# Kernel optimization log

Hardware: AMD Instinct MI355X
Metric: run time of the kernel (lower is better)

The kernel has to match this reference:

```python
import jax, jax.numpy as jnp
import numpy as np

N_NODES = 262144
N_EDGES = 524288
N_GRAPHS = 8192
BN_EPS = 1e-5


def setup_inputs() -> dict:
    key = jax.random.key(0)
    ks = jax.random.split(key, 12)
    x = jax.random.normal(ks[0], (N_NODES, 77), dtype=jnp.float32)
    edge_index = jax.random.randint(ks[1], (2, N_EDGES), 0, N_NODES, dtype=jnp.int32)
    # sorted segment ids covering every graph (arange-style fill)
    batch = (jnp.arange(N_NODES, dtype=jnp.int32) * N_GRAPHS // N_NODES).astype(jnp.int32)
    s77 = 1.0 / np.sqrt(77.0)
    s128 = 1.0 / np.sqrt(128.0)
    return {
        "x": x,
        "edge_index": edge_index,
        "batch": batch,
        "w0a": jax.random.normal(ks[2], (77, 128), dtype=jnp.float32) * s77,
        "b0a": jnp.zeros((128,), jnp.float32),
        "w0b": jax.random.normal(ks[3], (128, 128), dtype=jnp.float32) * s128,
        "b0b": jnp.zeros((128,), jnp.float32),
        "wa": jax.random.normal(ks[4], (4, 128, 128), dtype=jnp.float32) * s128,
        "ba": jnp.zeros((4, 128), jnp.float32),
        "wb": jax.random.normal(ks[5], (4, 128, 128), dtype=jnp.float32) * s128,
        "bb": jnp.zeros((4, 128), jnp.float32),
        "gamma": jnp.ones((5, 128), jnp.float32),
        "beta": jnp.zeros((5, 128), jnp.float32),
    }


def _gin_encoder(x, edge_index, batch, w0a, b0a, w0b, b0b, wa, ba, wb, bb, gamma, beta):
    n = x.shape[0]
    src, dst = edge_index[0], edge_index[1]
    h = x
    pooled = []
    for i in range(5):
        # GINConv (eps=0): agg_i = h_i + sum_{(j,i) in E} h_j, then 2-layer MLP
        agg = h + jax.ops.segment_sum(h[src], dst, num_segments=n)
        if i == 0:
            w1, c1, w2, c2 = w0a, b0a, w0b, b0b
        else:
            w1, c1, w2, c2 = wa[i - 1], ba[i - 1], wb[i - 1], bb[i - 1]
        h = jax.nn.relu(agg @ w1 + c1) @ w2 + c2
        h = jax.nn.relu(h)
        # BatchNorm1d (training-mode batch statistics, biased variance)
        mean = jnp.mean(h, axis=0)
        var = jnp.mean(jnp.square(h - mean), axis=0)
        h = gamma[i] * (h - mean) * jax.lax.rsqrt(var + BN_EPS) + beta[i]
        pooled.append(jax.ops.segment_max(h, batch, num_segments=N_GRAPHS))
    return jnp.concatenate(pooled, axis=1)  # [N_GRAPHS, 640]


def reference(x, edge_index, batch, w0a, b0a, w0b, b0b, wa, ba, wb, bb, gamma, beta):
    return _gin_encoder(x, edge_index, batch, w0a, b0a, w0b, b0b, wa, ba, wb, bb, gamma, beta)
```

## Files before the change

kernel.cpp:

```cpp
#include <hip/hip_runtime.h>
#include <cstdint>
#include <cstddef>

#define N_NODES_C 262144
#define N_EDGES_C 524288
#define N_GRAPHS_C 8192
#define BN_EPS_C 1e-5f

typedef short short8 __attribute__((ext_vector_type(8)));
typedef float f32x4 __attribute__((ext_vector_type(4)));

__device__ __forceinline__ unsigned short f2bf(float f) {
  unsigned int u = __float_as_uint(f);
  u += 0x7fffu + ((u >> 16) & 1u);
  return (unsigned short)(u >> 16);
}
__device__ __forceinline__ float bf2f(unsigned short h) {
  return __uint_as_float(((unsigned int)h) << 16);
}

__global__ __launch_bounds__(256) void hist_kernel(const int* __restrict__ dst, int* __restrict__ cnt) {
  int e = blockIdx.x * 256 + threadIdx.x;
  if (e < N_EDGES_C) atomicAdd(&cnt[dst[e]], 1);
}

__global__ __launch_bounds__(256) void scanA_kernel(const int* __restrict__ cnt,
                                                    int* __restrict__ rs, int* __restrict__ bsums) {
  __shared__ int lds[256];
  const int b = blockIdx.x, t = threadIdx.x;
  int4 v = ((const int4*)(cnt + b * 1024))[t];
  lds[t] = v.x + v.y + v.z + v.w;
  __syncthreads();
  for (int off = 1; off < 256; off <<= 1) {
    int add = (t >= off) ? lds[t - off] : 0;
    __syncthreads();
    lds[t] += add;
    __syncthreads();
  }
  int excl = (t > 0) ? lds[t - 1] : 0;
  if (t == 255) bsums[b] = lds[255];
  int4 o;
  o.x = excl; o.y = excl + v.x; o.z = excl + v.x + v.y; o.w = excl + v.x + v.y + v.z;
  ((int4*)(rs + b * 1024))[t] = o;
}

__global__ __launch_bounds__(256) void scanB_kernel(int* __restrict__ bsums) {
  __shared__ int lds[256];
  const int t = threadIdx.x;
  lds[t] = bsums[t];
  __syncthreads();
  for (int off = 1; off < 256; off <<= 1) {
    int add = (t >= off) ? lds[t - off] : 0;
    __syncthreads();
    lds[t] += add;
    __syncthreads();
  }
  bsums[t] = (t > 0) ? lds[t - 1] : 0;
}

__global__ __launch_bounds__(256) void scanC_kernel(int* __restrict__ rs, int* __restrict__ cursor,
                                                    const int* __restrict__ bsums) {
  int i = blockIdx.x * 256 + threadIdx.x;
  int v = rs[i] + bsums[i >> 10];
  rs[i] = v;
  cursor[i] = v;
  if (i == 0) rs[N_NODES_C] = N_EDGES_C;
}

__global__ __launch_bounds__(256) void edge_bucket_kernel(const int* __restrict__ src,
                                                          const int* __restrict__ dst,
                                                          int* __restrict__ cursor,
                                                          int* __restrict__ ebuf) {
  int e = blockIdx.x * 256 + threadIdx.x;
  if (e >= N_EDGES_C) return;
  int pos = atomicAdd(&cursor[dst[e]], 1);
  ebuf[pos] = src[e];
}

__global__ __launch_bounds__(256) void agg128_kernel(const float4* __restrict__ h4,
                                                     const int* __restrict__ rs,
                                                     const int* __restrict__ ebuf,
                                                     float4* __restrict__ agg4) {
  int idx = blockIdx.x * 256 + threadIdx.x;
  int n = idx >> 5, q = idx & 31;
  int s = rs[n], e = rs[n + 1];
  float4 v = h4[(size_t)n * 32 + q];
  for (int i = s; i < e; ++i) {
    int srcn = ebuf[i];
    float4 u = h4[(size_t)srcn * 32 + q];
    v.x += u.x; v.y += u.y; v.z += u.z; v.w += u.w;
  }
  agg4[(size_t)n * 32 + q] = v;
}

__global__ __launch_bounds__(256) void agg77_kernel(const float* __restrict__ x,
                                                    const int* __restrict__ rs,
                                                    const int* __restrict__ ebuf,
                                                    float* __restrict__ agg) {
  int idx = blockIdx.x * 256 + threadIdx.x;
  int n = idx >> 5, q = idx & 31;
  int s = rs[n], e = rs[n + 1];
  const size_t nb = (size_t)n * 77;
  float v0 = x[nb + q];
  float v1 = x[nb + q + 32];
  float v2 = (q < 13) ? x[nb + q + 64] : 0.f;
  for (int i = s; i < e; ++i) {
    const size_t sb = (size_t)ebuf[i] * 77;
    v0 += x[sb + q];
    v1 += x[sb + q + 32];
    if (q < 13) v2 += x[sb + q + 64];
  }
  const size_t ob = (size_t)n * 128;
  agg[ob + q] = v0;
  agg[ob + q + 32] = v1;
  agg[ob + q + 64] = (q < 13) ? v2 : 0.f;
  agg[ob + q + 96] = 0.f;
}

__global__ __launch_bounds__(256) void wsplit_kernel(const float* __restrict__ w0a,
                                                     const float* __restrict__ w0b,
                                                     const float* __restrict__ wa,
                                                     const float* __restrict__ wb,
                                                     unsigned short* __restrict__ Whi,
                                                     unsigned short* __restrict__ Wlo) {
  int tid = blockIdx.x * 256 + threadIdx.x;
  int mat = tid >> 11;
  int rem = tid & 2047;
  int ct = rem >> 8;
  int ks = (rem >> 6) & 3;
  int lane = rem & 63;
  const int c = ct * 16 + (lane & 15);
  const size_t base = (size_t)mat * 16384 + (size_t)((ct * 4 + ks) * 64 + lane) * 8;
#pragma unroll
  for (int j = 0; j < 8; ++j) {
    int k = ks * 32 + ((lane >> 4) << 3) + j;
    float w;
    if (mat == 0)      w = (k < 77) ? w0a[k * 128 + c] : 0.f;
    else if (mat == 1) w = w0b[k * 128 + c];
    else if (mat < 6)  w = wa[(size_t)(mat - 2) * 16384 + k * 128 + c];
    else               w = wb[(size_t)(mat - 6) * 16384 + k * 128 + c];
    unsigned short h = f2bf(w);
    Whi[base + j] = h;
    Wlo[base + j] = f2bf(w - bf2f(h));
  }
}

template <bool STATS>
__global__ __launch_bounds__(256) void gemm_kernel(const float* __restrict__ A,
                                                   const unsigned short* __restrict__ Whi,
                                                   const unsigned short* __restrict__ Wlo,
                                                   const float* __restrict__ bias,
                                                   float* __restrict__ C,
                                                   float* __restrict__ stats) {
  __shared__ float bsum[128];
  __shared__ float bsq[128];
  const int t = threadIdx.x;
  const int lane = t & 63;
  const int wv = t >> 6;
  if (STATS) {
    if (t < 128) { bsum[t] = 0.f; bsq[t] = 0.f; }
    __syncthreads();
  }

  const size_t strip = (size_t)blockIdx.x * 64 + wv * 16;
  const size_t rowA = strip + (lane & 15);
  const int kb = (lane >> 4) << 3;
  const float* Arow = A + rowA * 128 + kb;

  const short8* Bh = (const short8*)Whi;
  const short8* Bl = (const short8*)Wlo;

  f32x4 acc[8] = {};

#pragma unroll
  for (int ks = 0; ks < 4; ++ks) {
    f32x4 a0 = *(const f32x4*)(Arow + ks * 32);
    f32x4 a1 = *(const f32x4*)(Arow + ks * 32 + 4);
    short8 ah, al;
#pragma unroll
    for (int j = 0; j < 8; ++j) {
      float f = (j < 4) ? a0[j] : a1[j - 4];
      unsigned short h = f2bf(f);
      ah[j] = (short)h;
      al[j] = (short)f2bf(f - bf2f(h));
    }
#pragma unroll
    for (int ct = 0; ct < 8; ++ct) {
      const int idx = (ct * 4 + ks) * 64 + lane;
      short8 wh = Bh[idx];
      short8 wl = Bl[idx];
      acc[ct] = __builtin_amdgcn_mfma_f32_16x16x32_bf16(ah, wh, acc[ct], 0, 0, 0);
      acc[ct] = __builtin_amdgcn_mfma_f32_16x16x32_bf16(al, wh, acc[ct], 0, 0, 0);
      acc[ct] = __builtin_amdgcn_mfma_f32_16x16x32_bf16(ah, wl, acc[ct], 0, 0, 0);
    }
  }

  const int cbase = lane & 15;
  const size_t rowD = strip + ((lane >> 4) << 2);
#pragma unroll
  for (int ct = 0; ct < 8; ++ct) {
    const int c = ct * 16 + cbase;
    const float bc = bias[c];
    float s = 0.f, q = 0.f;
#pragma unroll
    for (int j = 0; j < 4; ++j) {
      float v = fmaxf(acc[ct][j] + bc, 0.f);
      C[(rowD + j) * 128 + c] = v;
      s += v;
      q += v * v;
    }
    if (STATS) {
      atomicAdd(&bsum[c], s);
      atomicAdd(&bsq[c], q);
    }
  }

  if (STATS) {
    __syncthreads();
    if (t < 128) {
      atomicAdd(&stats[t], bsum[t]);
      atomicAdd(&stats[128 + t], bsq[t]);
    }
  }
}

__global__ __launch_bounds__(256) void bn_pool_kernel(float* __restrict__ h,
                                                      const float* __restrict__ stats,
                                                      const float* __restrict__ gamma,
                                                      const float* __restrict__ beta,
                                                      float* __restrict__ out, int layer) {
  __shared__ float red[256];
  const int g = blockIdx.x;
  const int t = threadIdx.x;
  const int f = t & 127, half = t >> 7;

  const float inv_n = 1.0f / (float)N_NODES_C;
  float mean = stats[f] * inv_n;
  float var = stats[128 + f] * inv_n - mean * mean;
  float sc = gamma[layer * 128 + f] * rsqrtf(var + BN_EPS_C);
  float sh = beta[layer * 128 + f] - mean * sc;

  float m = -3.4e38f;
  size_t base = ((size_t)g * 32 + half * 16) * 128 + f;
#pragma unroll
  for (int r = 0; r < 16; ++r) {
    float v = h[base + (size_t)r * 128];
    v = v * sc + sh;
    h[base + (size_t)r * 128] = v;
    m = fmaxf(m, v);
  }
  red[t] = m;
  __syncthreads();
  if (t < 128) out[(size_t)g * 640 + layer * 128 + f] = fmaxf(red[t], red[t + 128]);
}

extern "C" void kernel_launch(void* const* d_in, const int* in_sizes, int n_in,
                              void* d_out, int out_size, void* d_ws, size_t ws_size,
                              hipStream_t stream) {
  const float* x = (const float*)d_in[0];
  const int* ei = (const int*)d_in[1];
  const int* src = ei;
  const int* dst = ei + N_EDGES_C;
  const float* w0a = (const float*)d_in[3];
  const float* b0a = (const float*)d_in[4];
  const float* w0b = (const float*)d_in[5];
  const float* b0b = (const float*)d_in[6];
  const float* wa = (const float*)d_in[7];
  const float* ba = (const float*)d_in[8];
  const float* wb = (const float*)d_in[9];
  const float* bb = (const float*)d_in[10];
  const float* gamma = (const float*)d_in[11];
  const float* beta = (const float*)d_in[12];
  float* out = (float*)d_out;

  const size_t NNf = (size_t)N_NODES_C * 128;
  float* ws = (float*)d_ws;
  float* H = ws;
  float* AGG = ws + NNf;
  float* STATS = ws + 2 * NNf;
  int* cnt = (int*)(STATS + 256);
  int* rowstart = cnt + N_NODES_C;
  int* cursor = rowstart + N_NODES_C + 4;
  int* bsums = cursor + N_NODES_C;
  int* ebuf = bsums + 256;
  unsigned short* Whi = (unsigned short*)(((uintptr_t)(ebuf + N_EDGES_C) + 15) & ~(uintptr_t)15);
  unsigned short* Wlo = Whi + (size_t)10 * 16384;

  wsplit_kernel<<<80, 256, 0, stream>>>(w0a, w0b, wa, wb, Whi, Wlo);
  hipMemsetAsync(cnt, 0, N_NODES_C * sizeof(int), stream);
  hist_kernel<<<N_EDGES_C / 256, 256, 0, stream>>>(dst, cnt);
  scanA_kernel<<<256, 256, 0, stream>>>(cnt, rowstart, bsums);
  scanB_kernel<<<1, 256, 0, stream>>>(bsums);
  scanC_kernel<<<N_NODES_C / 256, 256, 0, stream>>>(rowstart, cursor, bsums);
  edge_bucket_kernel<<<N_EDGES_C / 256, 256, 0, stream>>>(src, dst, cursor, ebuf);

  const int GB = N_NODES_C / 64;

  agg77_kernel<<<(N_NODES_C * 32) / 256, 256, 0, stream>>>(x, rowstart, ebuf, AGG);
  gemm_kernel<false><<<GB, 256, 0, stream>>>(AGG, Whi, Wlo, b0a, AGG, nullptr);
  hipMemsetAsync(STATS, 0, 256 * sizeof(float), stream);
  gemm_kernel<true><<<GB, 256, 0, stream>>>(AGG, Whi + 16384, Wlo + 16384, b0b, H, STATS);
  bn_pool_kernel<<<N_GRAPHS_C, 256, 0, stream>>>(H, STATS, gamma, beta, out, 0);

  for (int i = 1; i < 5; ++i) {
    agg128_kernel<<<(N_NODES_C * 32) / 256, 256, 0, stream>>>((const float4*)H, rowstart, ebuf,
                                                              (float4*)AGG);
    const size_t mA = (size_t)(2 + (i - 1)) * 16384;
    const size_t mB = (size_t)(6 + (i - 1)) * 16384;
    gemm_kernel<false><<<GB, 256, 0, stream>>>(AGG, Whi + mA, Wlo + mA,
                                               ba + (size_t)(i - 1) * 128, AGG, nullptr);
    hipMemsetAsync(STATS, 0, 256 * sizeof(float), stream);
    gemm_kernel<true><<<GB, 256, 0, stream>>>(AGG, Whi + mB, Wlo + mB,
                                              bb + (size_t)(i - 1) * 128, H, STATS);
    bn_pool_kernel<<<N_GRAPHS_C, 256, 0, stream>>>(H, STATS, gamma, beta, out, i);
  }
}
```

Baseline: 1.941 ms.

## Stage split-bf16 weights in LDS and process 512 rows per GEMM block

The GEMM kernel now copies the hi/lo bf16 weight matrices into 64 KB of shared memory once per block, instead of reading them from global or L2 for every 16-row strip. Each block covers 512 rows over four sub-blocks, with two 16-row tiles per wave so each weight fragment feeds six MFMAs. Batch-norm sums are kept in registers across the whole block and flushed once to shared and then global atomics, cutting atomic traffic. The trade-off is a grid of only 512 blocks and heavy LDS use, which lowers occupancy and latency hiding in this mostly bandwidth-bound GEMM.

```diff
diff --git a/kernel.cpp b/kernel.cpp
--- a/kernel.cpp
+++ b/kernel.cpp
@@ -152,70 +152,97 @@
                                                    const float* __restrict__ bias,
                                                    float* __restrict__ C,
                                                    float* __restrict__ stats) {
+  __shared__ int4 sW[4096];
   __shared__ float bsum[128];
   __shared__ float bsq[128];
+
   const int t = threadIdx.x;
   const int lane = t & 63;
   const int wv = t >> 6;
+
+  const int4* WhG = (const int4*)Whi;
+  const int4* WlG = (const int4*)Wlo;
+#pragma unroll
+  for (int i = 0; i < 8; ++i) sW[t + i * 256] = WhG[t + i * 256];
+#pragma unroll
+  for (int i = 0; i < 8; ++i) sW[2048 + t + i * 256] = WlG[t + i * 256];
+  __syncthreads();
+  const short8* sWh = (const short8*)sW;
+  const short8* sWl = (const short8*)(sW + 2048);
+
+  const int cbase = lane & 15;
+  const int kb = (lane >> 4) << 3;
+
+  float bc[8];
+#pragma unroll
+  for (int ct = 0; ct < 8; ++ct) bc[ct] = bias[ct * 16 + cbase];
+
+  float ssum[8] = {}, ssq[8] = {};
+
+  for (int sblk = 0; sblk < 4; ++sblk) {
+    const size_t strip = (size_t)blockIdx.x * 512 + sblk * 128 + wv * 32;
+    const float* Ar0 = A + (strip + cbase) * 128 + kb;
+    const float* Ar1 = Ar0 + 16 * 128;
+
+    f32x4 acc[2][8] = {};
+
+#pragma unroll
+    for (int ks = 0; ks < 4; ++ks) {
+      f32x4 a00 = *(const f32x4*)(Ar0 + ks * 32);
+      f32x4 a01 = *(const f32x4*)(Ar0 + ks * 32 + 4);
+      f32x4 a10 = *(const f32x4*)(Ar1 + ks * 32);
+      f32x4 a11 = *(const f32x4*)(Ar1 + ks * 32 + 4);
+      short8 ah0, al0, ah1, al1;
+#pragma unroll
+      for (int j = 0; j < 8; ++j) {
+        float f0 = (j < 4) ? a00[j] : a01[j - 4];
+        unsigned short h0 = f2bf(f0);
+        ah0[j] = (short)h0;
+        al0[j] = (short)f2bf(f0 - bf2f(h0));
+        float f1 = (j < 4) ? a10[j] : a11[j - 4];
+        unsigned short h1 = f2bf(f1);
+        ah1[j] = (short)h1;
+        al1[j] = (short)f2bf(f1 - bf2f(h1));
+      }
+#pragma unroll
+      for (int ct = 0; ct < 8; ++ct) {
+        const int idx = (ct * 4 + ks) * 64 + lane;
+        short8 wh = sWh[idx];
+        short8 wl = sWl[idx];
+        acc[0][ct] = __builtin_amdgcn_mfma_f32_16x16x32_bf16(ah0, wh, acc[0][ct], 0, 0, 0);
+        acc[0][ct] = __builtin_amdgcn_mfma_f32_16x16x32_bf16(al0, wh, acc[0][ct], 0, 0, 0);
+        acc[0][ct] = __builtin_amdgcn_mfma_f32_16x16x32_bf16(ah0, wl, acc[0][ct], 0, 0, 0);
+        acc[1][ct] = __builtin_amdgcn_mfma_f32_16x16x32_bf16(ah1, wh, acc[1][ct], 0, 0, 0);
+        acc[1][ct] = __builtin_amdgcn_mfma_f32_16x16x32_bf16(al1, wh, acc[1][ct], 0, 0, 0);
+        acc[1][ct] = __builtin_amdgcn_mfma_f32_16x16x32_bf16(ah1, wl, acc[1][ct], 0, 0, 0);
+      }
+    }
+
+#pragma unroll
+    for (int tile = 0; tile < 2; ++tile) {
+      const size_t rowD = strip + tile * 16 + ((lane >> 4) << 2);
+#pragma unroll
+      for (int ct = 0; ct < 8; ++ct) {
+        const int c = ct * 16 + cbase;
+#pragma unroll
+        for (int j = 0; j < 4; ++j) {
+          float v = fmaxf(acc[tile][ct][j] + bc[ct], 0.f);
+          C[(rowD + j) * 128 + c] = v;
+          if (STATS) { ssum[ct] += v; ssq[ct] += v * v; }
+        }
+      }
+    }
+  }
+
   if (STATS) {
     if (t < 128) { bsum[t] = 0.f; bsq[t] = 0.f; }
     __syncthreads();
-  }
-
-  const size_t strip = (size_t)blockIdx.x * 64 + wv * 16;
-  const size_t rowA = strip + (lane & 15);
-  const int kb = (lane >> 4) << 3;
-  const float* Arow = A + rowA * 128 + kb;
-
-  const short8* Bh = (const short8*)Whi;
-  const short8* Bl = (const short8*)Wlo;
-
-  f32x4 acc[8] = {};
-
-#pragma unroll
-  for (int ks = 0; ks < 4; ++ks) {
-    f32x4 a0 = *(const f32x4*)(Arow + ks * 32);
-    f32x4 a1 = *(const f32x4*)(Arow + ks * 32 + 4);
-    short8 ah, al;
-#pragma unroll
-    for (int j = 0; j < 8; ++j) {
-      float f = (j < 4) ? a0[j] : a1[j - 4];
-      unsigned short h = f2bf(f);
-      ah[j] = (short)h;
-      al[j] = (short)f2bf(f - bf2f(h));
+#pragma unroll
+    for (int ct = 0; ct < 8; ++ct) {
+      const int c = ct * 16 + cbase;
+      atomicAdd(&bsum[c], ssum[ct]);
+      atomicAdd(&bsq[c], ssq[ct]);
     }
-#pragma unroll
-    for (int ct = 0; ct < 8; ++ct) {
-      const int idx = (ct * 4 + ks) * 64 + lane;
-      short8 wh = Bh[idx];
-      short8 wl = Bl[idx];
-      acc[ct] = __builtin_amdgcn_mfma_f32_16x16x32_bf16(ah, wh, acc[ct], 0, 0, 0);
-      acc[ct] = __builtin_amdgcn_mfma_f32_16x16x32_bf16(al, wh, acc[ct], 0, 0, 0);
-      acc[ct] = __builtin_amdgcn_mfma_f32_16x16x32_bf16(ah, wl, acc[ct], 0, 0, 0);
-    }
-  }
-
-  const int cbase = lane & 15;
-  const size_t rowD = strip + ((lane >> 4) << 2);
-#pragma unroll
-  for (int ct = 0; ct < 8; ++ct) {
-    const int c = ct * 16 + cbase;
-    const float bc = bias[c];
-    float s = 0.f, q = 0.f;
-#pragma unroll
-    for (int j = 0; j < 4; ++j) {
-      float v = fmaxf(acc[ct][j] + bc, 0.f);
-      C[(rowD + j) * 128 + c] = v;
-      s += v;
-      q += v * v;
-    }
-    if (STATS) {
-      atomicAdd(&bsum[c], s);
-      atomicAdd(&bsq[c], q);
-    }
-  }
-
-  if (STATS) {
     __syncthreads();
     if (t < 128) {
       atomicAdd(&stats[t], bsum[t]);
@@ -294,7 +321,7 @@
   scanC_kernel<<<N_NODES_C / 256, 256, 0, stream>>>(rowstart, cursor, bsums);
   edge_bucket_kernel<<<N_EDGES_C / 256, 256, 0, stream>>>(src, dst, cursor, ebuf);
 
-  const int GB = N_NODES_C / 64;
+  const int GB = N_NODES_C / 512;
 
   agg77_kernel<<<(N_NODES_C * 32) / 256, 256, 0, stream>>>(x, rowstart, ebuf, AGG);
   gemm_kernel<false><<<GB, 256, 0, stream>>>(AGG, Whi, Wlo, b0a, AGG, nullptr);
```

Result: faster. 1.589 ms (-18.1%).

## Fuse gather, both MLP GEMMs and deferred BatchNorm into one layer kernel

Applied to the files above, without the earlier changes.

Replaces the per-layer sequence of aggregation, two GEMMs and a BN+pool kernel with a single fused kernel. It gathers neighbors, applies the previous layer's BatchNorm affine on the fly (scaled by neighbor count), runs both MLP GEMMs with the intermediate staged in swizzled LDS, and accumulates stats. Weights are packed for LDS staging, and the pool kernel no longer writes normalized H back. This removes several full passes over the 128 MB activation buffers. In exchange it launches only 256 blocks, reloads W1 into LDS every iteration, and uses large LDS and register footprints that may limit occupancy.

```diff
diff --git a/kernel.cpp b/kernel.cpp
--- a/kernel.cpp
+++ b/kernel.cpp
@@ -9,6 +9,8 @@
 
 typedef short short8 __attribute__((ext_vector_type(8)));
 typedef float f32x4 __attribute__((ext_vector_type(4)));
+
+union Frag { int2 p2[2]; short8 v8; };
 
 __device__ __forceinline__ unsigned short f2bf(float f) {
   unsigned int u = __float_as_uint(f);
@@ -75,22 +77,6 @@
   if (e >= N_EDGES_C) return;
   int pos = atomicAdd(&cursor[dst[e]], 1);
   ebuf[pos] = src[e];
-}
-
-__global__ __launch_bounds__(256) void agg128_kernel(const float4* __restrict__ h4,
-                                                     const int* __restrict__ rs,
-                                                     const int* __restrict__ ebuf,
-                                                     float4* __restrict__ agg4) {
-  int idx = blockIdx.x * 256 + threadIdx.x;
-  int n = idx >> 5, q = idx & 31;
-  int s = rs[n], e = rs[n + 1];
-  float4 v = h4[(size_t)n * 32 + q];
-  for (int i = s; i < e; ++i) {
-    int srcn = ebuf[i];
-    float4 u = h4[(size_t)srcn * 32 + q];
-    v.x += u.x; v.y += u.y; v.z += u.z; v.w += u.w;
-  }
-  agg4[(size_t)n * 32 + q] = v;
 }
 
 __global__ __launch_bounds__(256) void agg77_kernel(const float* __restrict__ x,
@@ -121,137 +107,258 @@
                                                      const float* __restrict__ w0b,
                                                      const float* __restrict__ wa,
                                                      const float* __restrict__ wb,
-                                                     unsigned short* __restrict__ Whi,
-                                                     unsigned short* __restrict__ Wlo) {
+                                                     unsigned short* __restrict__ Wpk) {
   int tid = blockIdx.x * 256 + threadIdx.x;
-  int mat = tid >> 11;
+  int m = tid >> 11;
   int rem = tid & 2047;
-  int ct = rem >> 8;
-  int ks = (rem >> 6) & 3;
-  int lane = rem & 63;
-  const int c = ct * 16 + (lane & 15);
-  const size_t base = (size_t)mat * 16384 + (size_t)((ct * 4 + ks) * 64 + lane) * 8;
+  int f = rem >> 6;
+  int l = rem & 63;
+  int ct = f >> 2, ks = f & 3;
+  int c = ct * 16 + (l & 15);
+  const size_t mb = (size_t)m * 32768;
+  const size_t fl = (size_t)(f * 64 + l) * 4;
 #pragma unroll
   for (int j = 0; j < 8; ++j) {
-    int k = ks * 32 + ((lane >> 4) << 3) + j;
+    int k = ks * 32 + ((l >> 4) << 3) + j;
     float w;
-    if (mat == 0)      w = (k < 77) ? w0a[k * 128 + c] : 0.f;
-    else if (mat == 1) w = w0b[k * 128 + c];
-    else if (mat < 6)  w = wa[(size_t)(mat - 2) * 16384 + k * 128 + c];
-    else               w = wb[(size_t)(mat - 6) * 16384 + k * 128 + c];
-    unsigned short h = f2bf(w);
-    Whi[base + j] = h;
-    Wlo[base + j] = f2bf(w - bf2f(h));
-  }
-}
-
-template <bool STATS>
-__global__ __launch_bounds__(256) void gemm_kernel(const float* __restrict__ A,
-                                                   const unsigned short* __restrict__ Whi,
-                                                   const unsigned short* __restrict__ Wlo,
-                                                   const float* __restrict__ bias,
-                                                   float* __restrict__ C,
-                                                   float* __restrict__ stats) {
+    if (m == 0)      w = (k < 77) ? w0a[k * 128 + c] : 0.f;
+    else if (m == 1) w = w0b[k * 128 + c];
+    else if (m < 6)  w = wa[(size_t)(m - 2) * 16384 + k * 128 + c];
+    else             w = wb[(size_t)(m - 6) * 16384 + k * 128 + c];
+    unsigned short hh = f2bf(w);
+    unsigned short ll = f2bf(w - bf2f(hh));
+    if (j < 4) {
+      Wpk[mb + fl + j] = hh;
+      Wpk[mb + 16384 + fl + j] = ll;
+    } else {
+      Wpk[mb + 8192 + fl + (j - 4)] = hh;
+      Wpk[mb + 24576 + fl + (j - 4)] = ll;
+    }
+  }
+}
+
+template <bool GATHER>
+__global__ __launch_bounds__(512, 2) void fused_layer_kernel(
+    const float* __restrict__ Hin,
+    const int* __restrict__ rs,
+    const int* __restrict__ ebuf,
+    const float* __restrict__ Sprev,
+    const float* __restrict__ gprev,
+    const float* __restrict__ bprev,
+    const unsigned short* __restrict__ W1pk,
+    const unsigned short* __restrict__ W2pk,
+    const float* __restrict__ b1,
+    const float* __restrict__ b2,
+    float* __restrict__ Hout,
+    float* __restrict__ Sout) {
+  __shared__ int4 sW2[4096];
+  __shared__ int4 sW1C[4096];
   __shared__ float bsum[128];
   __shared__ float bsq[128];
+
   const int t = threadIdx.x;
   const int lane = t & 63;
   const int wv = t >> 6;
-  if (STATS) {
-    if (t < 128) { bsum[t] = 0.f; bsq[t] = 0.f; }
-    __syncthreads();
-  }
-
-  const size_t strip = (size_t)blockIdx.x * 64 + wv * 16;
-  const size_t rowA = strip + (lane & 15);
-  const int kb = (lane >> 4) << 3;
-  const float* Arow = A + rowA * 128 + kb;
-
-  const short8* Bh = (const short8*)Whi;
-  const short8* Bl = (const short8*)Wlo;
-
-  f32x4 acc[8] = {};
-
-#pragma unroll
-  for (int ks = 0; ks < 4; ++ks) {
-    f32x4 a0 = *(const f32x4*)(Arow + ks * 32);
-    f32x4 a1 = *(const f32x4*)(Arow + ks * 32 + 4);
-    short8 ah, al;
-#pragma unroll
-    for (int j = 0; j < 8; ++j) {
-      float f = (j < 4) ? a0[j] : a1[j - 4];
-      unsigned short h = f2bf(f);
-      ah[j] = (short)h;
-      al[j] = (short)f2bf(f - bf2f(h));
-    }
+  const int cb = lane & 15;
+  const int g = lane >> 4;
+
+  {
+    const int4* s2 = (const int4*)W2pk;
+#pragma unroll
+    for (int i = 0; i < 8; ++i) sW2[t + i * 512] = s2[t + i * 512];
+  }
+
+  float bc1[8], bc2[8];
+#pragma unroll
+  for (int ct = 0; ct < 8; ++ct) {
+    bc1[ct] = b1[ct * 16 + cb];
+    bc2[ct] = b2[ct * 16 + cb];
+  }
+
+  f32x4 scv[8], shv[8];
+  if constexpr (GATHER) {
+    const float inv_n = 1.0f / (float)N_NODES_C;
+#pragma unroll
+    for (int q = 0; q < 8; ++q) {
+      int f0 = (q >> 1) * 32 + g * 8 + (q & 1) * 4;
+#pragma unroll
+      for (int j = 0; j < 4; ++j) {
+        int f = f0 + j;
+        float mean = Sprev[f] * inv_n;
+        float var = Sprev[128 + f] * inv_n - mean * mean;
+        float sc = gprev[f] * rsqrtf(var + BN_EPS_C);
+        scv[q][j] = sc;
+        shv[q][j] = bprev[f] - mean * sc;
+      }
+    }
+  }
+
+  float ssum[8] = {}, ssq[8] = {};
+  const size_t blockRow0 = (size_t)blockIdx.x * 1024;
+
+  for (int it = 0; it < 8; ++it) {
+    const size_t strip = blockRow0 + it * 128;
+    const size_t wrow0 = strip + wv * 16;
+
+    __syncthreads();
+    {
+      const int4* s1 = (const int4*)W1pk;
+#pragma unroll
+      for (int i = 0; i < 8; ++i) sW1C[t + i * 512] = s1[t + i * 512];
+    }
+
+    f32x4 va[8];
+    {
+      const size_t r = wrow0 + cb;
+      const float* hp = Hin + r * 128 + g * 8;
+#pragma unroll
+      for (int q = 0; q < 8; ++q)
+        va[q] = *(const f32x4*)(hp + (q >> 1) * 32 + (q & 1) * 4);
+      if constexpr (GATHER) {
+        int s = rs[r], e = rs[r + 1];
+        for (int i = s; i < e; ++i) {
+          const float* hq = Hin + (size_t)ebuf[i] * 128 + g * 8;
+#pragma unroll
+          for (int q = 0; q < 8; ++q)
+            va[q] += *(const f32x4*)(hq + (q >> 1) * 32 + (q & 1) * 4);
+        }
+        float cnt = (float)(e - s + 1);
+#pragma unroll
+        for (int q = 0; q < 8; ++q) va[q] = va[q] * scv[q] + cnt * shv[q];
+      }
+    }
+
+    Frag ah[4], al[4];
+#pragma unroll
+    for (int ks = 0; ks < 4; ++ks) {
+#pragma unroll
+      for (int j = 0; j < 8; ++j) {
+        float fv = va[ks * 2 + (j >> 2)][j & 3];
+        unsigned short hh = f2bf(fv);
+        ah[ks].v8[j] = (short)hh;
+        al[ks].v8[j] = (short)f2bf(fv - bf2f(hh));
+      }
+    }
+
+    __syncthreads();
+
+    f32x4 d1[8] = {};
+    {
+      const int2* R1 = (const int2*)sW1C;
+#pragma unroll
+      for (int ks = 0; ks < 4; ++ks) {
+#pragma unroll
+        for (int ct = 0; ct < 8; ++ct) {
+          int fi = (ct * 4 + ks) * 64 + lane;
+          Frag wh, wl;
+          wh.p2[0] = R1[fi];        wh.p2[1] = R1[2048 + fi];
+          wl.p2[0] = R1[4096 + fi]; wl.p2[1] = R1[6144 + fi];
+          d1[ct] = __builtin_amdgcn_mfma_f32_16x16x32_bf16(ah[ks].v8, wh.v8, d1[ct], 0, 0, 0);
+          d1[ct] = __builtin_amdgcn_mfma_f32_16x16x32_bf16(al[ks].v8, wh.v8, d1[ct], 0, 0, 0);
+          d1[ct] = __builtin_amdgcn_mfma_f32_16x16x32_bf16(ah[ks].v8, wl.v8, d1[ct], 0, 0, 0);
+        }
+      }
+    }
+    __syncthreads();
+
+    {
+      char* c1b = (char*)sW1C;
+#pragma unroll
+      for (int ct = 0; ct < 8; ++ct) {
+#pragma unroll
+        for (int j = 0; j < 4; ++j) {
+          int r = wv * 16 + g * 4 + j;
+          int c = ct * 16 + cb;
+          float v = fmaxf(d1[ct][j] + bc1[ct], 0.f);
+          *(float*)(c1b + ((r * 512 + c * 4) ^ ((r & 7) << 4))) = v;
+        }
+      }
+    }
+    __syncthreads();
+
+    f32x4 d2[8] = {};
+    {
+      const int rr = wv * 16 + cb;
+      const char* c1r = (const char*)sW1C;
+      const int2* R2 = (const int2*)sW2;
+#pragma unroll
+      for (int ks = 0; ks < 4; ++ks) {
+        int base = rr * 512 + ks * 128 + g * 32;
+        f32x4 x0 = *(const f32x4*)(c1r + ((base) ^ ((rr & 7) << 4)));
+        f32x4 x1 = *(const f32x4*)(c1r + ((base + 16) ^ ((rr & 7) << 4)));
+        Frag a2h, a2l;
+#pragma unroll
+        for (int j = 0; j < 8; ++j) {
+          float fv = (j < 4) ? x0[j] : x1[j - 4];
+          unsigned short hh = f2bf(fv);
+          a2h.v8[j] = (short)hh;
+          a2l.v8[j] = (short)f2bf(fv - bf2f(hh));
+        }
+#pragma unroll
+        for (int ct = 0; ct < 8; ++ct) {
+          int fi = (ct * 4 + ks) * 64 + lane;
+          Frag wh, wl;
+          wh.p2[0] = R2[fi];        wh.p2[1] = R2[2048 + fi];
+          wl.p2[0] = R2[4096 + fi]; wl.p2[1] = R2[6144 + fi];
+          d2[ct] = __builtin_amdgcn_mfma_f32_16x16x32_bf16(a2h.v8, wh.v8, d2[ct], 0, 0, 0);
+          d2[ct] = __builtin_amdgcn_mfma_f32_16x16x32_bf16(a2l.v8, wh.v8, d2[ct], 0, 0, 0);
+          d2[ct] = __builtin_amdgcn_mfma_f32_16x16x32_bf16(a2h.v8, wl.v8, d2[ct], 0, 0, 0);
+        }
+      }
+    }
+
 #pragma unroll
     for (int ct = 0; ct < 8; ++ct) {
-      const int idx = (ct * 4 + ks) * 64 + lane;
-      short8 wh = Bh[idx];
-      short8 wl = Bl[idx];
-      acc[ct] = __builtin_amdgcn_mfma_f32_16x16x32_bf16(ah, wh, acc[ct], 0, 0, 0);
-      acc[ct] = __builtin_amdgcn_mfma_f32_16x16x32_bf16(al, wh, acc[ct], 0, 0, 0);
-      acc[ct] = __builtin_amdgcn_mfma_f32_16x16x32_bf16(ah, wl, acc[ct], 0, 0, 0);
-    }
-  }
-
-  const int cbase = lane & 15;
-  const size_t rowD = strip + ((lane >> 4) << 2);
+      const int c = ct * 16 + cb;
+#pragma unroll
+      for (int j = 0; j < 4; ++j) {
+        size_t r = wrow0 + g * 4 + j;
+        float v = fmaxf(d2[ct][j] + bc2[ct], 0.f);
+        Hout[r * 128 + c] = v;
+        ssum[ct] += v;
+        ssq[ct] += v * v;
+      }
+    }
+  }
+
+  if (t < 128) { bsum[t] = 0.f; bsq[t] = 0.f; }
+  __syncthreads();
 #pragma unroll
   for (int ct = 0; ct < 8; ++ct) {
-    const int c = ct * 16 + cbase;
-    const float bc = bias[c];
-    float s = 0.f, q = 0.f;
-#pragma unroll
-    for (int j = 0; j < 4; ++j) {
-      float v = fmaxf(acc[ct][j] + bc, 0.f);
-      C[(rowD + j) * 128 + c] = v;
-      s += v;
-      q += v * v;
-    }
-    if (STATS) {
-      atomicAdd(&bsum[c], s);
-      atomicAdd(&bsq[c], q);
-    }
-  }
-
-  if (STATS) {
-    __syncthreads();
-    if (t < 128) {
-      atomicAdd(&stats[t], bsum[t]);
-      atomicAdd(&stats[128 + t], bsq[t]);
-    }
-  }
-}
-
-__global__ __launch_bounds__(256) void bn_pool_kernel(float* __restrict__ h,
-                                                      const float* __restrict__ stats,
-                                                      const float* __restrict__ gamma,
-                                                      const float* __restrict__ beta,
-                                                      float* __restrict__ out, int layer) {
+    atomicAdd(&bsum[ct * 16 + cb], ssum[ct]);
+    atomicAdd(&bsq[ct * 16 + cb], ssq[ct]);
+  }
+  __syncthreads();
+  if (t < 128) {
+    atomicAdd(&Sout[t], bsum[t]);
+    atomicAdd(&Sout[128 + t], bsq[t]);
+  }
+}
+
+__global__ __launch_bounds__(256) void pool_kernel(const float* __restrict__ h,
+                                                   const float* __restrict__ stats,
+                                                   const float* __restrict__ gamma,
+                                                   const float* __restrict__ beta,
+                                                   float* __restrict__ out, int layer) {
   __shared__ float red[256];
-  const int g = blockIdx.x;
+  const int gph = blockIdx.x;
   const int t = threadIdx.x;
   const int f = t & 127, half = t >> 7;
 
   const float inv_n = 1.0f / (float)N_NODES_C;
   float mean = stats[f] * inv_n;
   float var = stats[128 + f] * inv_n - mean * mean;
-  float sc = gamma[layer * 128 + f] * rsqrtf(var + BN_EPS_C);
-  float sh = beta[layer * 128 + f] - mean * sc;
+  float sc = gamma[f] * rsqrtf(var + BN_EPS_C);
+  float sh = beta[f] - mean * sc;
 
   float m = -3.4e38f;
-  size_t base = ((size_t)g * 32 + half * 16) * 128 + f;
-#pragma unroll
-  for (int r = 0; r < 16; ++r) {
-    float v = h[base + (size_t)r * 128];
-    v = v * sc + sh;
-    h[base + (size_t)r * 128] = v;
-    m = fmaxf(m, v);
-  }
+  size_t base = ((size_t)gph * 32 + half * 16) * 128 + f;
+#pragma unroll
+  for (int r = 0; r < 16; ++r)
+    m = fmaxf(m, h[base + (size_t)r * 128] * sc + sh);
   red[t] = m;
   __syncthreads();
-  if (t < 128) out[(size_t)g * 640 + layer * 128 + f] = fmaxf(red[t], red[t + 128]);
+  if (t < 128) out[(size_t)gph * 640 + layer * 128 + f] = fmaxf(red[t], red[t + 128]);
 }
 
 extern "C" void kernel_launch(void* const* d_in, const int* in_sizes, int n_in,
@@ -275,43 +382,43 @@
 
   const size_t NNf = (size_t)N_NODES_C * 128;
   float* ws = (float*)d_ws;
-  float* H = ws;
-  float* AGG = ws + NNf;
+  float* Hb0 = ws;
+  float* Hb1 = ws + NNf;
   float* STATS = ws + 2 * NNf;
-  int* cnt = (int*)(STATS + 256);
+  int* cnt = (int*)(STATS + 5 * 256);
   int* rowstart = cnt + N_NODES_C;
   int* cursor = rowstart + N_NODES_C + 4;
   int* bsums = cursor + N_NODES_C;
   int* ebuf = bsums + 256;
-  unsigned short* Whi = (unsigned short*)(((uintptr_t)(ebuf + N_EDGES_C) + 15) & ~(uintptr_t)15);
-  unsigned short* Wlo = Whi + (size_t)10 * 16384;
-
-  wsplit_kernel<<<80, 256, 0, stream>>>(w0a, w0b, wa, wb, Whi, Wlo);
+  unsigned short* Wpk = (unsigned short*)(((uintptr_t)(ebuf + N_EDGES_C) + 63) & ~(uintptr_t)63);
+
+  wsplit_kernel<<<80, 256, 0, stream>>>(w0a, w0b, wa, wb, Wpk);
   hipMemsetAsync(cnt, 0, N_NODES_C * sizeof(int), stream);
+  hipMemsetAsync(STATS, 0, 5 * 256 * sizeof(float), stream);
   hist_kernel<<<N_EDGES_C / 256, 256, 0, stream>>>(dst, cnt);
   scanA_kernel<<<256, 256, 0, stream>>>(cnt, rowstart, bsums);
   scanB_kernel<<<1, 256, 0, stream>>>(bsums);
   scanC_kernel<<<N_NODES_C / 256, 256, 0, stream>>>(rowstart, cursor, bsums);
   edge_bucket_kernel<<<N_EDGES_C / 256, 256, 0, stream>>>(src, dst, cursor, ebuf);
 
-  const int GB = N_NODES_C / 64;
-
-  agg77_kernel<<<(N_NODES_C * 32) / 256, 256, 0, stream>>>(x, rowstart, ebuf, AGG);
-  gemm_kernel<false><<<GB, 256, 0, stream>>>(AGG, Whi, Wlo, b0a, AGG, nullptr);
-  hipMemsetAsync(STATS, 0, 256 * sizeof(float), stream);
-  gemm_kernel<true><<<GB, 256, 0, stream>>>(AGG, Whi + 16384, Wlo + 16384, b0b, H, STATS);
-  bn_pool_kernel<<<N_GRAPHS_C, 256, 0, stream>>>(H, STATS, gamma, beta, out, 0);
-
+  agg77_kernel<<<(N_NODES_C * 32) / 256, 256, 0, stream>>>(x, rowstart, ebuf, Hb1);
+  fused_layer_kernel<false><<<256, 512, 0, stream>>>(
+      Hb1, rowstart, ebuf, nullptr, nullptr, nullptr,
+      Wpk + 0 * 32768, Wpk + 1 * 32768, b0a, b0b, Hb0, STATS + 0 * 256);
+  pool_kernel<<<N_GRAPHS_C, 256, 0, stream>>>(Hb0, STATS + 0 * 256, gamma, beta, out, 0);
+
+  float* cur = Hb0;
+  float* nxt = Hb1;
   for (int i = 1; i < 5; ++i) {
-    agg128_kernel<<<(N_NODES_C * 32) / 256, 256, 0, stream>>>((const float4*)H, rowstart, ebuf,
-                                                              (float4*)AGG);
-    const size_t mA = (size_t)(2 + (i - 1)) * 16384;
-    const size_t mB = (size_t)(6 + (i - 1)) * 16384;
-    gemm_kernel<false><<<GB, 256, 0, stream>>>(AGG, Whi + mA, Wlo + mA,
-                                               ba + (size_t)(i - 1) * 128, AGG, nullptr);
-    hipMemsetAsync(STATS, 0, 256 * sizeof(float), stream);
-    gemm_kernel<true><<<GB, 256, 0, stream>>>(AGG, Whi + mB, Wlo + mB,
-                                              bb + (size_t)(i - 1) * 128, H, STATS);
-    bn_pool_kernel<<<N_GRAPHS_C, 256, 0, stream>>>(H, STATS, gamma, beta, out, i);
-  }
-}
+    fused_layer_kernel<true><<<256, 512, 0, stream>>>(
+        cur, rowstart, ebuf,
+        STATS + (size_t)(i - 1) * 256, gamma + (size_t)(i - 1) * 128, beta + (size_t)(i - 1) * 128,
+        Wpk + (size_t)(2 + (i - 1)) * 32768, Wpk + (size_t)(6 + (i - 1)) * 32768,
+        ba + (size_t)(i - 1) * 128, bb + (size_t)(i - 1) * 128,
+        nxt, STATS + (size_t)i * 256);
+    pool_kernel<<<N_GRAPHS_C, 256, 0, stream>>>(nxt, STATS + (size_t)i * 256,
+                                                gamma + (size_t)i * 128, beta + (size_t)i * 128,
+                                                out, i);
+    float* tmp = cur; cur = nxt; nxt = tmp;
+  }
+}
```

Result: faster. 1.706 ms (-12.1%).
